# Kernel optimization log

Hardware: AMD Instinct MI355X
Metric: run time of the kernel (lower is better)

## Reference

```python
import jax, jax.numpy as jnp
import numpy as np

B, S, D = 4, 1024, 1024
H, DK, DH = 16, 64, 64  # num_heads, key_size, head_size
NEG = 1e12


def setup_inputs() -> dict:
    key = jax.random.key(0)
    ks = jax.random.split(key, 16)
    scale = 0.02
    inp = {
        'q': jax.random.normal(ks[0], (B, S, D), jnp.float32),
        'k': jax.random.normal(ks[1], (B, S, D), jnp.float32),
        'v': jax.random.normal(ks[2], (B, S, D), jnp.float32),
        'v_mask': jax.random.randint(ks[3], (B, S), 0, 2, jnp.int32),
        'q_mask': jax.random.randint(ks[4], (B, S), 0, 2, jnp.int32),
        # causal attention mask (float, 1 = keep)
        'a_mask': jnp.tril(jnp.ones((S, S), jnp.float32))[None, None, :, :],
        'Wq': jax.random.normal(ks[5], (D, H * DK), jnp.float32) * scale,
        'bq': jnp.zeros((H * DK,), jnp.float32),
        'Wk': jax.random.normal(ks[6], (D, H * DK), jnp.float32) * scale,
        'bk': jnp.zeros((H * DK,), jnp.float32),
        'Wv': jax.random.normal(ks[7], (D, H * DH), jnp.float32) * scale,
        'bv': jnp.zeros((H * DH,), jnp.float32),
        'Wo': jax.random.normal(ks[8], (H * DH, H * DH), jnp.float32) * scale,
        'bo': jnp.zeros((H * DH,), jnp.float32),
    }
    return inp


def reference(q, k, v, v_mask, q_mask, a_mask, Wq, bq, Wk, bk, Wv, bv, Wo, bo):
    b, sq, _ = q.shape
    sk = k.shape[1]
    qw = (jnp.einsum('bsd,de->bse', q, Wq) + bq).reshape(b, sq, H, DK)
    kw = (jnp.einsum('bsd,de->bse', k, Wk) + bk).reshape(b, sk, H, DK)
    vw = (jnp.einsum('bsd,de->bse', v, Wv) + bv).reshape(b, sk, H, DH)
    # scores [b, h, sq, sk]
    a = jnp.einsum('bjhd,bkhd->bhjk', qw, kw) / jnp.sqrt(jnp.float32(DK))
    vm = v_mask.astype(jnp.float32)  # [b, sk]
    a = a - (1.0 - vm)[:, None, None, :] * NEG  # sequence_masking mode='add'
    a = a - (1.0 - a_mask) * NEG                # attention mask
    p = jax.nn.softmax(a, axis=-1)
    o = jnp.einsum('bhjk,bkhd->bjhd', p, vw).reshape(b, sq, H * DH)
    o = jnp.einsum('bse,ef->bsf', o, Wo) + bo
    qm = q_mask.astype(jnp.float32)
    o = o * qm[:, :, None]  # sequence_masking mode='mul'
    return o
```

## Files before the change

kernel.cpp:

```cpp
#include <hip/hip_runtime.h>
#include <cstdint>
#include <cstddef>

typedef unsigned short u16;
using short8 = __attribute__((ext_vector_type(8))) short;
using f32x4  = __attribute__((ext_vector_type(4))) float;

constexpr int Sc = 1024;
constexpr float PEN = 60.0f;

__device__ __forceinline__ u16 f2bf(float f) {
  union { float f; uint32_t u; } v; v.f = f;
  return (u16)((v.u + 0x7fffu + ((v.u >> 16) & 1u)) >> 16);
}

__device__ __forceinline__ void gload_lds16(const u16* g, u16* l) {
  __builtin_amdgcn_global_load_lds(
      (const __attribute__((address_space(1))) uint32_t*)g,
      (__attribute__((address_space(3))) uint32_t*)l, 16, 0, 0);
}

__device__ __forceinline__ f32x4 mfma16(short8 a, short8 b, f32x4 c) {
  return __builtin_amdgcn_mfma_f32_16x16x32_bf16(a, b, c, 0, 0, 0);
}

__global__ __launch_bounds__(256) void cvt3(const float* __restrict__ q,
                                            const float* __restrict__ k,
                                            const float* __restrict__ v,
                                            u16* __restrict__ qb,
                                            u16* __restrict__ kb,
                                            u16* __restrict__ vb) {
  const float* src = blockIdx.y == 0 ? q : blockIdx.y == 1 ? k : v;
  u16* dst = blockIdx.y == 0 ? qb : blockIdx.y == 1 ? kb : vb;
  int i = blockIdx.x * 256 + threadIdx.x;
  float4 a = ((const float4*)src)[2 * i];
  float4 b = ((const float4*)src)[2 * i + 1];
  u16 t[8] = {f2bf(a.x), f2bf(a.y), f2bf(a.z), f2bf(a.w),
              f2bf(b.x), f2bf(b.y), f2bf(b.z), f2bf(b.w)};
  ((uint4*)dst)[i] = *(const uint4*)t;
}

__global__ __launch_bounds__(256) void transpose_cvt4(
    const float* __restrict__ W0, const float* __restrict__ W1,
    const float* __restrict__ W2, const float* __restrict__ W3,
    u16* __restrict__ D0, u16* __restrict__ D1, u16* __restrict__ D2,
    u16* __restrict__ D3) {
  const float* W = blockIdx.z == 0 ? W0 : blockIdx.z == 1 ? W1
                 : blockIdx.z == 2 ? W2 : W3;
  u16* WT = blockIdx.z == 0 ? D0 : blockIdx.z == 1 ? D1
          : blockIdx.z == 2 ? D2 : D3;
  __shared__ float t[32][33];
  int bx = blockIdx.x * 32, by = blockIdx.y * 32;
  int tx = threadIdx.x & 31, ty = threadIdx.x >> 5;
  for (int i = 0; i < 32; i += 8)
    t[ty + i][tx] = W[(size_t)(by + ty + i) * 1024 + bx + tx];
  __syncthreads();
  for (int i = 0; i < 32; i += 8)
    WT[(size_t)(bx + ty + i) * 1024 + by + tx] = f2bf(t[tx][ty + i]);
}

__global__ __launch_bounds__(256) void gemm_qkv(
    const u16* __restrict__ qb, const u16* __restrict__ kb,
    const u16* __restrict__ vb, const u16* __restrict__ BT,
    const float* __restrict__ bq, const float* __restrict__ bk,
    const float* __restrict__ bv, u16* __restrict__ QW, u16* __restrict__ KW,
    u16* __restrict__ VTg) {
  const int n0 = blockIdx.x * 128, m0 = blockIdx.y * 128;
  const int seg = n0 >> 10;
  const u16* A    = seg == 0 ? qb : seg == 1 ? kb : vb;
  const float* bias = seg == 0 ? bq : seg == 1 ? bk : bv;

  __shared__ u16 As[128 * 32];
  __shared__ u16 Bs[128 * 32];

  const int t = threadIdx.x, w = t >> 6, lane = t & 63;
  const int q4 = lane >> 4, lm = lane & 15;
  const int wm = (w >> 1) * 64, wn = (w & 1) * 64;
  const int srow = lane >> 2, p = lane & 3;

  f32x4 acc[4][4] = {};

  for (int k0 = 0; k0 < 1024; k0 += 32) {
    __syncthreads();
    for (int j = 0; j < 2; ++j) {
      const int rbase = (w * 2 + j) * 16;
      const int row = rbase + srow;
      const int c = p ^ ((row >> 2) & 3);
      gload_lds16(&A[(size_t)(m0 + row) * 1024 + k0 + c * 8], &As[rbase * 32]);
      gload_lds16(&BT[(size_t)(n0 + row) * 1024 + k0 + c * 8], &Bs[rbase * 32]);
    }
    __syncthreads();
    short8 af[4], bf[4];
    for (int mi = 0; mi < 4; ++mi) {
      int row = wm + mi * 16 + lm;
      af[mi] = *(const short8*)&As[row * 32 + ((q4 ^ ((row >> 2) & 3)) * 8)];
    }
    for (int ni = 0; ni < 4; ++ni) {
      int row = wn + ni * 16 + lm;
      bf[ni] = *(const short8*)&Bs[row * 32 + ((q4 ^ ((row >> 2) & 3)) * 8)];
    }
    for (int mi = 0; mi < 4; ++mi)
      for (int ni = 0; ni < 4; ++ni)
        acc[mi][ni] = mfma16(af[mi], bf[ni], acc[mi][ni]);
  }
  if (seg < 2) {
    u16* C = seg == 0 ? QW : KW;
    for (int mi = 0; mi < 4; ++mi)
      for (int ni = 0; ni < 4; ++ni)
        for (int r = 0; r < 4; ++r) {
          int row = m0 + wm + mi * 16 + q4 * 4 + r;
          int col = (n0 + wn + ni * 16 + lm) & 1023;
          C[(size_t)row * 1024 + col] = f2bf(acc[mi][ni][r] + bias[col]);
        }
  } else {
    for (int mi = 0; mi < 4; ++mi)
      for (int ni = 0; ni < 4; ++ni) {
        int row0 = m0 + wm + mi * 16 + q4 * 4;
        int col = (n0 + wn + ni * 16 + lm) & 1023;
        float bv4 = bias[col];
        u16 o4[4];
        for (int r = 0; r < 4; ++r) o4[r] = f2bf(acc[mi][ni][r] + bv4);
        *(uint2*)&VTg[(size_t)col * 4096 + row0] = *(const uint2*)o4;
      }
  }
}

__global__ __launch_bounds__(256) void gemm_out(
    const u16* __restrict__ A, const u16* __restrict__ BT,
    const float* __restrict__ bias, const int* __restrict__ qmask,
    float* __restrict__ Cf) {
  const int n0 = blockIdx.x * 128, m0 = blockIdx.y * 128;
  __shared__ u16 As[128 * 32];
  __shared__ u16 Bs[128 * 32];
  const int t = threadIdx.x, w = t >> 6, lane = t & 63;
  const int q4 = lane >> 4, lm = lane & 15;
  const int wm = (w >> 1) * 64, wn = (w & 1) * 64;
  const int srow = lane >> 2, p = lane & 3;
  f32x4 acc[4][4] = {};
  for (int k0 = 0; k0 < 1024; k0 += 32) {
    __syncthreads();
    for (int j = 0; j < 2; ++j) {
      const int rbase = (w * 2 + j) * 16;
      const int row = rbase + srow;
      const int c = p ^ ((row >> 2) & 3);
      gload_lds16(&A[(size_t)(m0 + row) * 1024 + k0 + c * 8], &As[rbase * 32]);
      gload_lds16(&BT[(size_t)(n0 + row) * 1024 + k0 + c * 8], &Bs[rbase * 32]);
    }
    __syncthreads();
    short8 af[4], bf[4];
    for (int mi = 0; mi < 4; ++mi) {
      int row = wm + mi * 16 + lm;
      af[mi] = *(const short8*)&As[row * 32 + ((q4 ^ ((row >> 2) & 3)) * 8)];
    }
    for (int ni = 0; ni < 4; ++ni) {
      int row = wn + ni * 16 + lm;
      bf[ni] = *(const short8*)&Bs[row * 32 + ((q4 ^ ((row >> 2) & 3)) * 8)];
    }
    for (int mi = 0; mi < 4; ++mi)
      for (int ni = 0; ni < 4; ++ni)
        acc[mi][ni] = mfma16(af[mi], bf[ni], acc[mi][ni]);
  }
  for (int mi = 0; mi < 4; ++mi)
    for (int ni = 0; ni < 4; ++ni)
      for (int r = 0; r < 4; ++r) {
        int row = m0 + wm + mi * 16 + q4 * 4 + r;
        int col = n0 + wn + ni * 16 + lm;
        Cf[(size_t)row * 1024 + col] =
            (acc[mi][ni][r] + bias[col]) * (float)qmask[row];
      }
}

__global__ __launch_bounds__(256) void attn(
    const u16* __restrict__ QW, const u16* __restrict__ KW,
    const u16* __restrict__ VTg, const int* __restrict__ vmask,
    u16* __restrict__ O) {
  const int bx = blockIdx.x, h = blockIdx.y, b = blockIdx.z;
  const int qta = bx, qtb = 15 - bx;
  const int t = threadIdx.x, w = t >> 6, lane = t & 63;
  const int q4 = lane >> 4, lm = lane & 15;

  __shared__ u16 Ks[2][64 * 64];
  __shared__ u16 VTs[2][64 * 64];
  __shared__ u16 P[4][16 * 88];
  __shared__ float penv[1024];
  __shared__ int anyf[2];

  if (t < 2) anyf[t] = 0;
  {
    int4 vm = ((const int4*)(vmask + b * 1024))[t];
    penv[4 * t + 0] = (1.f - (float)vm.x) * PEN;
    penv[4 * t + 1] = (1.f - (float)vm.y) * PEN;
    penv[4 * t + 2] = (1.f - (float)vm.z) * PEN;
    penv[4 * t + 3] = (1.f - (float)vm.w) * PEN;
  }
  __syncthreads();
  {
    int any_a = 0, any_b = 0;
    for (int i = t; i <= qtb * 64; i += 256) {
      int un = (penv[i] == 0.f);
      if (i <= qta * 64) any_a |= un;
      any_b |= un;
    }
    if (any_a) atomicOr(&anyf[0], 1);
    if (any_b) atomicOr(&anyf[1], 1);
  }
  __syncthreads();
  const int extA = !anyf[0], extB = !anyf[1];
  const int kend = (extA || extB) ? 15 : qtb;

  short8 qf[2][2];
  for (int s = 0; s < 2; ++s) {
    int qt = s ? qtb : qta;
    const u16* qp = &QW[(size_t)(b * Sc + qt * 64 + w * 16 + lm) * 1024 + h * 64];
    qf[s][0] = *(const short8*)&qp[q4 * 8];
    qf[s][1] = *(const short8*)&qp[32 + q4 * 8];
    for (int fi = 0; fi < 2; ++fi)
      for (int i = 0; i < 8; ++i) {
        u16 x = (u16)qf[s][fi][i];
        int e = (x >> 7) & 0xff;
        qf[s][fi][i] = (short)(e > 3 ? (u16)(x - 0x180) : (u16)(x & 0x8000));
      }
  }

  float l_run[2][4] = {};
  f32x4 oacc[2][4] = {};

  const int r0 = lane >> 3, pos = lane & 7, ch = pos ^ r0;
  auto stage = [&](int kt, int buf) {
    for (int j = 0; j < 2; ++j) {
      int issue = w * 2 + j;
      int row = issue * 8 + r0;
      gload_lds16(&KW[(size_t)(b * Sc + kt * 64 + row) * 1024 + h * 64 + ch * 8],
                  &Ks[buf][issue * 512]);
      gload_lds16(&VTg[(size_t)(h * 64 + row) * 4096 + b * Sc + kt * 64 + ch * 8],
                  &VTs[buf][issue * 512]);
    }
  };

  auto strip_tile = [&](int s, int kt, int mode, int buf) {
    const int qt = s ? qtb : qta;
    const int qrow0 = qt * 64 + w * 16 + q4 * 4;
    f32x4 sacc[4] = {};
    for (int ni = 0; ni < 4; ++ni) {
      int row = ni * 16 + lm;
      short8 kf0 = *(const short8*)&Ks[buf][row * 64 + ((q4 ^ (lm & 7)) * 8)];
      short8 kf1 = *(const short8*)&Ks[buf][row * 64 + (((4 + q4) ^ (lm & 7)) * 8)];
      sacc[ni] = mfma16(qf[s][0], kf0, sacc[ni]);
      sacc[ni] = mfma16(qf[s][1], kf1, sacc[ni]);
    }
    u16* Pw = &P[w][0];
    for (int ni = 0; ni < 4; ++ni) {
      int key = kt * 64 + ni * 16 + lm;
      float pen = penv[key];
      if (mode == 2) pen += PEN;
      for (int r = 0; r < 4; ++r) {
        float x = sacc[ni][r] - pen;
        if (mode == 1 && key > qrow0 + r) x -= PEN;
        float pv = __expf(x);
        l_run[s][r] += pv;
        Pw[(q4 * 4 + r) * 88 + ni * 16 + lm] = f2bf(pv);
      }
    }
    short8 pf0 = *(const short8*)&Pw[lm * 88 + q4 * 8];
    short8 pf1 = *(const short8*)&Pw[lm * 88 + 32 + q4 * 8];
    for (int ni = 0; ni < 4; ++ni) {
      int row = ni * 16 + lm;
      short8 vf0 = *(const short8*)&VTs[buf][row * 64 + ((q4 ^ (lm & 7)) * 8)];
      short8 vf1 = *(const short8*)&VTs[buf][row * 64 + (((4 + q4) ^ (lm & 7)) * 8)];
      oacc[s][ni] = mfma16(pf0, vf0, oacc[s][ni]);
      oacc[s][ni] = mfma16(pf1, vf1, oacc[s][ni]);
    }
  };

  stage(0, 0);
  int cur = 0;
  for (int kt = 0; kt <= kend; ++kt) {
    __syncthreads();
    if (kt < kend) stage(kt + 1, cur ^ 1);
    if (kt <= qta) strip_tile(0, kt, kt == qta ? 1 : 0, cur);
    else if (extA) strip_tile(0, kt, 2, cur);
    if (kt <= qtb) strip_tile(1, kt, kt == qtb ? 1 : 0, cur);
    else if (extB) strip_tile(1, kt, 2, cur);
    cur ^= 1;
  }

  for (int s = 0; s < 2; ++s) {
    int qt = s ? qtb : qta;
    for (int r = 0; r < 4; ++r) {
      float l = l_run[s][r];
      for (int off = 1; off < 16; off <<= 1) l += __shfl_xor(l, off, 64);
      l_run[s][r] = 1.0f / l;
    }
    for (int ni = 0; ni < 4; ++ni)
      for (int r = 0; r < 4; ++r) {
        int row = b * Sc + qt * 64 + w * 16 + q4 * 4 + r;
        O[(size_t)row * 1024 + h * 64 + ni * 16 + lm] =
            f2bf(oacc[s][ni][r] * l_run[s][r]);
      }
  }
}

extern "C" void kernel_launch(void* const* d_in, const int* in_sizes, int n_in,
                              void* d_out, int out_size, void* d_ws, size_t ws_size,
                              hipStream_t stream) {
  (void)in_sizes; (void)n_in; (void)out_size; (void)ws_size;
  const float* q  = (const float*)d_in[0];
  const float* k  = (const float*)d_in[1];
  const float* v  = (const float*)d_in[2];
  const int* vmask = (const int*)d_in[3];
  const int* qmask = (const int*)d_in[4];
  const float* Wq = (const float*)d_in[6];
  const float* bq = (const float*)d_in[7];
  const float* Wk = (const float*)d_in[8];
  const float* bk = (const float*)d_in[9];
  const float* Wv = (const float*)d_in[10];
  const float* bv = (const float*)d_in[11];
  const float* Wo = (const float*)d_in[12];
  const float* bo = (const float*)d_in[13];

  char* ws = (char*)d_ws;
  u16* WT3 = (u16*)ws;
  u16* WoT = (u16*)(ws + 6291456);
  u16* QW  = (u16*)(ws + 8388608);
  u16* KW  = (u16*)(ws + 16777216);
  u16* VTg = (u16*)(ws + 25165824);
  u16* Oat = (u16*)(ws + 33554432);
  u16* qb = (u16*)d_out;
  u16* kb = (u16*)d_out + 4194304;
  u16* vb = Oat;

  dim3 tb(256);
  transpose_cvt4<<<dim3(32, 32, 4), tb, 0, stream>>>(
      Wq, Wk, Wv, Wo, WT3, WT3 + 1048576, WT3 + 2097152, WoT);
  cvt3<<<dim3(2048, 3), tb, 0, stream>>>(q, k, v, qb, kb, vb);
  gemm_qkv<<<dim3(24, 32), tb, 0, stream>>>(qb, kb, vb, WT3, bq, bk, bv, QW,
                                            KW, VTg);
  attn<<<dim3(8, 16, 4), tb, 0, stream>>>(QW, KW, VTg, vmask, Oat);
  gemm_out<<<dim3(8, 32), tb, 0, stream>>>(Oat, WoT, bo, qmask, (float*)d_out);
}
```

Before: 248.8 us.

## Double-buffer LDS in projection GEMMs and halve output GEMM M-tile

Both GEMM kernels now use two LDS buffers. The next K-slice is staged with global_load_lds while the current slice is being consumed by MFMA, which cuts the barriers to one per iteration and overlaps load latency with compute. The output projection GEMM also drops its M tile from 128 to 64 rows, doubling the block count to fill more CUs. The cost is a larger LDS footprint and smaller per-block reuse in the output GEMM, and correctness depends on the barrier waiting for the async LDS loads.

```diff
diff --git a/kernel.cpp b/kernel.cpp
--- a/kernel.cpp
+++ b/kernel.cpp
@@ -70,39 +70,44 @@
   const u16* A    = seg == 0 ? qb : seg == 1 ? kb : vb;
   const float* bias = seg == 0 ? bq : seg == 1 ? bk : bv;
 
-  __shared__ u16 As[128 * 32];
-  __shared__ u16 Bs[128 * 32];
+  __shared__ u16 As[2][128 * 32];
+  __shared__ u16 Bs[2][128 * 32];
 
   const int t = threadIdx.x, w = t >> 6, lane = t & 63;
   const int q4 = lane >> 4, lm = lane & 15;
   const int wm = (w >> 1) * 64, wn = (w & 1) * 64;
   const int srow = lane >> 2, p = lane & 3;
+  const int cs = p ^ ((srow >> 2) & 3);
+  const int cf = q4 ^ ((lm >> 2) & 3);
 
   f32x4 acc[4][4] = {};
 
-  for (int k0 = 0; k0 < 1024; k0 += 32) {
+  auto stage = [&](int k0, int buf) {
+    for (int j = 0; j < 2; ++j) {
+      const int issue = w * 2 + j;
+      const int row = issue * 16 + srow;
+      gload_lds16(&A[(size_t)(m0 + row) * 1024 + k0 + cs * 8],
+                  &As[buf][issue * 512]);
+      gload_lds16(&BT[(size_t)(n0 + row) * 1024 + k0 + cs * 8],
+                  &Bs[buf][issue * 512]);
+    }
+  };
+
+  stage(0, 0);
+  for (int it = 0; it < 32; ++it) {
+    const int buf = it & 1;
     __syncthreads();
-    for (int j = 0; j < 2; ++j) {
-      const int rbase = (w * 2 + j) * 16;
-      const int row = rbase + srow;
-      const int c = p ^ ((row >> 2) & 3);
-      gload_lds16(&A[(size_t)(m0 + row) * 1024 + k0 + c * 8], &As[rbase * 32]);
-      gload_lds16(&BT[(size_t)(n0 + row) * 1024 + k0 + c * 8], &Bs[rbase * 32]);
-    }
-    __syncthreads();
+    if (it < 31) stage((it + 1) * 32, buf ^ 1);
     short8 af[4], bf[4];
-    for (int mi = 0; mi < 4; ++mi) {
-      int row = wm + mi * 16 + lm;
-      af[mi] = *(const short8*)&As[row * 32 + ((q4 ^ ((row >> 2) & 3)) * 8)];
-    }
-    for (int ni = 0; ni < 4; ++ni) {
-      int row = wn + ni * 16 + lm;
-      bf[ni] = *(const short8*)&Bs[row * 32 + ((q4 ^ ((row >> 2) & 3)) * 8)];
-    }
+    for (int mi = 0; mi < 4; ++mi)
+      af[mi] = *(const short8*)&As[buf][(wm + mi * 16 + lm) * 32 + cf * 8];
+    for (int ni = 0; ni < 4; ++ni)
+      bf[ni] = *(const short8*)&Bs[buf][(wn + ni * 16 + lm) * 32 + cf * 8];
     for (int mi = 0; mi < 4; ++mi)
       for (int ni = 0; ni < 4; ++ni)
         acc[mi][ni] = mfma16(af[mi], bf[ni], acc[mi][ni]);
   }
+
   if (seg < 2) {
     u16* C = seg == 0 ? QW : KW;
     for (int mi = 0; mi < 4; ++mi)
@@ -129,38 +134,48 @@
     const u16* __restrict__ A, const u16* __restrict__ BT,
     const float* __restrict__ bias, const int* __restrict__ qmask,
     float* __restrict__ Cf) {
-  const int n0 = blockIdx.x * 128, m0 = blockIdx.y * 128;
-  __shared__ u16 As[128 * 32];
-  __shared__ u16 Bs[128 * 32];
+  const int n0 = blockIdx.x * 128, m0 = blockIdx.y * 64;
+  __shared__ u16 As[2][64 * 32];
+  __shared__ u16 Bs[2][128 * 32];
   const int t = threadIdx.x, w = t >> 6, lane = t & 63;
   const int q4 = lane >> 4, lm = lane & 15;
-  const int wm = (w >> 1) * 64, wn = (w & 1) * 64;
+  const int wm = (w >> 1) * 32, wn = (w & 1) * 64;
   const int srow = lane >> 2, p = lane & 3;
-  f32x4 acc[4][4] = {};
-  for (int k0 = 0; k0 < 1024; k0 += 32) {
+  const int cs = p ^ ((srow >> 2) & 3);
+  const int cf = q4 ^ ((lm >> 2) & 3);
+
+  f32x4 acc[2][4] = {};
+
+  auto stage = [&](int k0, int buf) {
+    {
+      const int row = w * 16 + srow;
+      gload_lds16(&A[(size_t)(m0 + row) * 1024 + k0 + cs * 8],
+                  &As[buf][w * 512]);
+    }
+    for (int j = 0; j < 2; ++j) {
+      const int issue = w * 2 + j;
+      const int row = issue * 16 + srow;
+      gload_lds16(&BT[(size_t)(n0 + row) * 1024 + k0 + cs * 8],
+                  &Bs[buf][issue * 512]);
+    }
+  };
+
+  stage(0, 0);
+  for (int it = 0; it < 32; ++it) {
+    const int buf = it & 1;
     __syncthreads();
-    for (int j = 0; j < 2; ++j) {
-      const int rbase = (w * 2 + j) * 16;
-      const int row = rbase + srow;
-      const int c = p ^ ((row >> 2) & 3);
-      gload_lds16(&A[(size_t)(m0 + row) * 1024 + k0 + c * 8], &As[rbase * 32]);
-      gload_lds16(&BT[(size_t)(n0 + row) * 1024 + k0 + c * 8], &Bs[rbase * 32]);
-    }
-    __syncthreads();
-    short8 af[4], bf[4];
-    for (int mi = 0; mi < 4; ++mi) {
-      int row = wm + mi * 16 + lm;
-      af[mi] = *(const short8*)&As[row * 32 + ((q4 ^ ((row >> 2) & 3)) * 8)];
-    }
-    for (int ni = 0; ni < 4; ++ni) {
-      int row = wn + ni * 16 + lm;
-      bf[ni] = *(const short8*)&Bs[row * 32 + ((q4 ^ ((row >> 2) & 3)) * 8)];
-    }
-    for (int mi = 0; mi < 4; ++mi)
+    if (it < 31) stage((it + 1) * 32, buf ^ 1);
+    short8 af[2], bf[4];
+    for (int mi = 0; mi < 2; ++mi)
+      af[mi] = *(const short8*)&As[buf][(wm + mi * 16 + lm) * 32 + cf * 8];
+    for (int ni = 0; ni < 4; ++ni)
+      bf[ni] = *(const short8*)&Bs[buf][(wn + ni * 16 + lm) * 32 + cf * 8];
+    for (int mi = 0; mi < 2; ++mi)
       for (int ni = 0; ni < 4; ++ni)
         acc[mi][ni] = mfma16(af[mi], bf[ni], acc[mi][ni]);
   }
-  for (int mi = 0; mi < 4; ++mi)
+
+  for (int mi = 0; mi < 2; ++mi)
     for (int ni = 0; ni < 4; ++ni)
       for (int r = 0; r < 4; ++r) {
         int row = m0 + wm + mi * 16 + q4 * 4 + r;
@@ -336,5 +351,5 @@
   gemm_qkv<<<dim3(24, 32), tb, 0, stream>>>(qb, kb, vb, WT3, bq, bk, bv, QW,
                                             KW, VTg);
   attn<<<dim3(8, 16, 4), tb, 0, stream>>>(QW, KW, VTg, vmask, Oat);
-  gemm_out<<<dim3(8, 32), tb, 0, stream>>>(Oat, WoT, bo, qmask, (float*)d_out);
-}
+  gemm_out<<<dim3(8, 64), tb, 0, stream>>>(Oat, WoT, bo, qmask, (float*)d_out);
+}
```

Result: slower. 256.1 us (+2.9%).

## Remap block indices for XCD-aware L2 locality and shrink output GEMM tile

Applied to the files above, without the earlier changes.

Flattens the grids of the QKV GEMM, attention and output GEMM into 1D and remaps block IDs so that blocks landing on the same XCD (round-robin by bid&7) share the same A rows or batch-head pairs, aiming to improve per-XCD L2 reuse. The output GEMM tile shrinks from 128x128 to 64x128, doubling its block count to 512 for better occupancy across CUs, at the cost of less register reuse per block. The LDS swizzle column computation is also hoisted out of the loop.

```diff
diff --git a/kernel.cpp b/kernel.cpp
--- a/kernel.cpp
+++ b/kernel.cpp
@@ -65,8 +65,11 @@
     const float* __restrict__ bq, const float* __restrict__ bk,
     const float* __restrict__ bv, u16* __restrict__ QW, u16* __restrict__ KW,
     u16* __restrict__ VTg) {
-  const int n0 = blockIdx.x * 128, m0 = blockIdx.y * 128;
-  const int seg = n0 >> 10;
+  const int bid = blockIdx.x;
+  const int xcd = bid & 7, local = bid >> 3;
+  const int mp = local & 3, nbi = local >> 2;
+  const int m0 = (xcd * 4 + mp) * 128, n0 = nbi * 128;
+  const int seg = nbi >> 3;
   const u16* A    = seg == 0 ? qb : seg == 1 ? kb : vb;
   const float* bias = seg == 0 ? bq : seg == 1 ? bk : bv;
 
@@ -77,6 +80,7 @@
   const int q4 = lane >> 4, lm = lane & 15;
   const int wm = (w >> 1) * 64, wn = (w & 1) * 64;
   const int srow = lane >> 2, p = lane & 3;
+  const int cf = q4 ^ ((lm >> 2) & 3);
 
   f32x4 acc[4][4] = {};
 
@@ -91,14 +95,10 @@
     }
     __syncthreads();
     short8 af[4], bf[4];
-    for (int mi = 0; mi < 4; ++mi) {
-      int row = wm + mi * 16 + lm;
-      af[mi] = *(const short8*)&As[row * 32 + ((q4 ^ ((row >> 2) & 3)) * 8)];
-    }
-    for (int ni = 0; ni < 4; ++ni) {
-      int row = wn + ni * 16 + lm;
-      bf[ni] = *(const short8*)&Bs[row * 32 + ((q4 ^ ((row >> 2) & 3)) * 8)];
-    }
+    for (int mi = 0; mi < 4; ++mi)
+      af[mi] = *(const short8*)&As[(wm + mi * 16 + lm) * 32 + cf * 8];
+    for (int ni = 0; ni < 4; ++ni)
+      bf[ni] = *(const short8*)&Bs[(wn + ni * 16 + lm) * 32 + cf * 8];
     for (int mi = 0; mi < 4; ++mi)
       for (int ni = 0; ni < 4; ++ni)
         acc[mi][ni] = mfma16(af[mi], bf[ni], acc[mi][ni]);
@@ -129,38 +129,46 @@
     const u16* __restrict__ A, const u16* __restrict__ BT,
     const float* __restrict__ bias, const int* __restrict__ qmask,
     float* __restrict__ Cf) {
-  const int n0 = blockIdx.x * 128, m0 = blockIdx.y * 128;
-  __shared__ u16 As[128 * 32];
+  const int bid = blockIdx.x;
+  const int xcd = bid & 7, local = bid >> 3;
+  const int mp = local & 7, nb = local >> 3;
+  const int m0 = (xcd * 8 + mp) * 64, n0 = nb * 128;
+
+  __shared__ u16 As[64 * 32];
   __shared__ u16 Bs[128 * 32];
   const int t = threadIdx.x, w = t >> 6, lane = t & 63;
   const int q4 = lane >> 4, lm = lane & 15;
-  const int wm = (w >> 1) * 64, wn = (w & 1) * 64;
+  const int wm = (w >> 1) * 32, wn = (w & 1) * 64;
   const int srow = lane >> 2, p = lane & 3;
-  f32x4 acc[4][4] = {};
+  const int cf = q4 ^ ((lm >> 2) & 3);
+
+  f32x4 acc[2][4] = {};
+
   for (int k0 = 0; k0 < 1024; k0 += 32) {
     __syncthreads();
+    {
+      const int row = w * 16 + srow;
+      const int c = p ^ ((row >> 2) & 3);
+      gload_lds16(&A[(size_t)(m0 + row) * 1024 + k0 + c * 8], &As[w * 512]);
+    }
     for (int j = 0; j < 2; ++j) {
       const int rbase = (w * 2 + j) * 16;
       const int row = rbase + srow;
       const int c = p ^ ((row >> 2) & 3);
-      gload_lds16(&A[(size_t)(m0 + row) * 1024 + k0 + c * 8], &As[rbase * 32]);
       gload_lds16(&BT[(size_t)(n0 + row) * 1024 + k0 + c * 8], &Bs[rbase * 32]);
     }
     __syncthreads();
-    short8 af[4], bf[4];
-    for (int mi = 0; mi < 4; ++mi) {
-      int row = wm + mi * 16 + lm;
-      af[mi] = *(const short8*)&As[row * 32 + ((q4 ^ ((row >> 2) & 3)) * 8)];
-    }
-    for (int ni = 0; ni < 4; ++ni) {
-      int row = wn + ni * 16 + lm;
-      bf[ni] = *(const short8*)&Bs[row * 32 + ((q4 ^ ((row >> 2) & 3)) * 8)];
-    }
-    for (int mi = 0; mi < 4; ++mi)
+    short8 af[2], bf[4];
+    for (int mi = 0; mi < 2; ++mi)
+      af[mi] = *(const short8*)&As[(wm + mi * 16 + lm) * 32 + cf * 8];
+    for (int ni = 0; ni < 4; ++ni)
+      bf[ni] = *(const short8*)&Bs[(wn + ni * 16 + lm) * 32 + cf * 8];
+    for (int mi = 0; mi < 2; ++mi)
       for (int ni = 0; ni < 4; ++ni)
         acc[mi][ni] = mfma16(af[mi], bf[ni], acc[mi][ni]);
   }
-  for (int mi = 0; mi < 4; ++mi)
+
+  for (int mi = 0; mi < 2; ++mi)
     for (int ni = 0; ni < 4; ++ni)
       for (int r = 0; r < 4; ++r) {
         int row = m0 + wm + mi * 16 + q4 * 4 + r;
@@ -174,7 +182,11 @@
     const u16* __restrict__ QW, const u16* __restrict__ KW,
     const u16* __restrict__ VTg, const int* __restrict__ vmask,
     u16* __restrict__ O) {
-  const int bx = blockIdx.x, h = blockIdx.y, b = blockIdx.z;
+  const int bid = blockIdx.x;
+  const int xcd = bid & 7, local = bid >> 3;
+  const int pair = xcd * 8 + (local & 7);
+  const int b = pair >> 4, h = pair & 15;
+  const int bx = local >> 3;
   const int qta = bx, qtb = 15 - bx;
   const int t = threadIdx.x, w = t >> 6, lane = t & 63;
   const int q4 = lane >> 4, lm = lane & 15;
@@ -333,8 +345,8 @@
   transpose_cvt4<<<dim3(32, 32, 4), tb, 0, stream>>>(
       Wq, Wk, Wv, Wo, WT3, WT3 + 1048576, WT3 + 2097152, WoT);
   cvt3<<<dim3(2048, 3), tb, 0, stream>>>(q, k, v, qb, kb, vb);
-  gemm_qkv<<<dim3(24, 32), tb, 0, stream>>>(qb, kb, vb, WT3, bq, bk, bv, QW,
-                                            KW, VTg);
-  attn<<<dim3(8, 16, 4), tb, 0, stream>>>(QW, KW, VTg, vmask, Oat);
-  gemm_out<<<dim3(8, 32), tb, 0, stream>>>(Oat, WoT, bo, qmask, (float*)d_out);
-}
+  gemm_qkv<<<dim3(768), tb, 0, stream>>>(qb, kb, vb, WT3, bq, bk, bv, QW, KW,
+                                         VTg);
+  attn<<<dim3(512), tb, 0, stream>>>(QW, KW, VTg, vmask, Oat);
+  gemm_out<<<dim3(512), tb, 0, stream>>>(Oat, WoT, bo, qmask, (float*)d_out);
+}
```

After: 234.6 us. -5.7%, faster.
